# Optimization experiments

Measured on AMD Instinct MI355X. Metric: run time of the kernel, lower is better.

## Reference

```python
import jax, jax.numpy as jnp
import numpy as np

H = 1024
NH = 16
B = 32
S = 4096


def setup_inputs() -> dict:
    key = jax.random.key(0)
    ks = jax.random.split(key, 9)
    std = 0.02
    return {
        "x": jax.random.normal(ks[0], (B, S, H), dtype=jnp.float32),
        "Wq": jax.random.normal(ks[1], (H, H), dtype=jnp.float32) * std,
        "bq": jax.random.normal(ks[2], (H,), dtype=jnp.float32) * std,
        "Wk": jax.random.normal(ks[3], (H, H), dtype=jnp.float32) * std,
        "bk": jax.random.normal(ks[4], (H,), dtype=jnp.float32) * std,
        "Wv": jax.random.normal(ks[5], (H, H), dtype=jnp.float32) * std,
        "bv": jax.random.normal(ks[6], (H,), dtype=jnp.float32) * std,
        "Wo": jax.random.normal(ks[7], (H, H), dtype=jnp.float32) * std,
        "bo": jax.random.normal(ks[8], (H,), dtype=jnp.float32) * std,
        "n_heads": NH,
    }


def reference(x, Wq, bq, Wk, bk, Wv, bv, Wo, bo, n_heads):
    b, s, h = x.shape
    dk = h // n_heads
    scale = dk ** -0.5
    # Q only from last position (decode-style single query)
    q = (x[:, -1, :] @ Wq.T + bq).reshape(b, n_heads, dk)          # (B,H,dk)
    k = (x @ Wk.T + bk).reshape(b, s, n_heads, dk)                 # (B,S,H,dk)
    v = (x @ Wv.T + bv).reshape(b, s, n_heads, dk)
    scores = jnp.einsum('bhd,bshd->bhs', q, k) * scale             # (B,H,S)
    attn = jax.nn.softmax(scores, axis=-1)
    out = jnp.einsum('bhs,bshd->bhd', attn, v).reshape(b, h)       # (B,hidden)
    return out @ Wo.T + bo
```

## Files before the change

kernel.cpp:

```cpp
#include <hip/hip_runtime.h>
#include <hip/hip_bf16.h>

#define B_  32
#define S_  4096
#define H_  1024
#define NH_ 16
#define DK_ 64
#define NCH 32
#define ROWS 128
#define TILE 4
#define NT (ROWS / TILE)

#define Q_OFF  0
#define T_OFF  (Q_OFF + B_*H_)
#define YP_OFF (T_OFF + B_*NH_*H_)
#define ML_OFF (YP_OFF + NCH*B_*NH_*H_)
#define Y2_OFF (ML_OFF + NCH*B_*2*NH_)
#define OP_OFF (Y2_OFF + B_*NH_*H_)

#define DOT4(a, v) ((a).x*(v).x + (a).y*(v).y + (a).z*(v).z + (a).w*(v).w)

typedef float v2f __attribute__((ext_vector_type(2)));
struct alignas(16) F4 { v2f lo, hi; };

__device__ __forceinline__ v2f v2z() { v2f z; z.x = 0.f; z.y = 0.f; return z; }

template <int CTRL>
__device__ __forceinline__ float dppadd(float v) {
  int mv = __builtin_amdgcn_update_dpp(0, __float_as_int(v), CTRL, 0xF, 0xF, true);
  return v + __int_as_float(mv);
}

__global__ __launch_bounds__(256) void k_q(const float* __restrict__ x,
                                           const float* __restrict__ Wq,
                                           const float* __restrict__ bq,
                                           float* __restrict__ q) {
  __shared__ __align__(16) float xl[4 * H_];
  int islab = blockIdx.x, bg = blockIdx.y, tid = threadIdx.x;
  #pragma unroll
  for (int k = 0; k < 4; ++k) {
    int idx4 = k * 256 + tid;
    int bl = idx4 >> 8, col4 = idx4 & 255;
    *(float4*)&xl[bl * H_ + col4 * 4] =
        *(const float4*)(x + (((size_t)(bg * 4 + bl)) * S_ + (S_ - 1)) * H_ + col4 * 4);
  }
  __syncthreads();
  int d = tid >> 2, p = tid & 3;
  int i = islab * 64 + d;
  const float* w = Wq + (size_t)i * H_ + p * 256;
  float acc[4] = {0.f, 0.f, 0.f, 0.f};
  #pragma unroll 4
  for (int jj = 0; jj < 256; jj += 4) {
    float4 wv = *(const float4*)(w + jj);
    #pragma unroll
    for (int bl = 0; bl < 4; ++bl) {
      float4 xv = *(const float4*)&xl[bl * H_ + p * 256 + jj];
      acc[bl] += DOT4(xv, wv);
    }
  }
  #pragma unroll
  for (int bl = 0; bl < 4; ++bl) {
    acc[bl] += __shfl_xor(acc[bl], 1);
    acc[bl] += __shfl_xor(acc[bl], 2);
  }
  if (p == 0) {
    float bias = bq[i];
    #pragma unroll
    for (int bl = 0; bl < 4; ++bl)
      q[(size_t)(bg * 4 + bl) * H_ + i] = acc[bl] + bias;
  }
}

__global__ __launch_bounds__(256) void k_t(const float* __restrict__ q,
                                           const float* __restrict__ Wk,
                                           float* __restrict__ t) {
  __shared__ __align__(16) float qh[B_ * DK_];
  int js = blockIdx.x, h = blockIdx.y, tid = threadIdx.x;
  #pragma unroll
  for (int k = 0; k < 2; ++k) {
    int idx4 = k * 256 + tid;
    int bl = idx4 >> 4, d4 = idx4 & 15;
    *(float4*)&qh[bl * DK_ + d4 * 4] =
        *(const float4*)(q + (size_t)bl * H_ + h * DK_ + d4 * 4);
  }
  __syncthreads();

  int bh = tid >> 7;
  int j = js * 128 + (tid & 127);
  float acc[16];
  #pragma unroll
  for (int bl = 0; bl < 16; ++bl) acc[bl] = 0.f;
  for (int d = 0; d < DK_; ++d) {
    float wv = Wk[((size_t)(h * DK_ + d)) * H_ + j];
    #pragma unroll
    for (int bl = 0; bl < 16; ++bl) acc[bl] += qh[(bh * 16 + bl) * DK_ + d] * wv;
  }
  #pragma unroll
  for (int bl = 0; bl < 16; ++bl)
    t[((size_t)((bh * 16 + bl) * NH_ + h)) * H_ + j] = acc[bl];
}

__global__ __launch_bounds__(256) void k_flash(const float* __restrict__ x,
                                               const float* __restrict__ t,
                                               float* __restrict__ ypart,
                                               float* __restrict__ mlpart) {
  int ch = blockIdx.x, b = blockIdx.y, tid = threadIdx.x;
  int wv = tid >> 6, ln = tid & 63;

  const float* xg = x + ((size_t)b * S_ + (size_t)ch * ROWS) * H_ + ln * 16;

  F4 tf[4][4];
  #pragma unroll
  for (int hh = 0; hh < 4; ++hh) {
    const float* tg = t + ((size_t)b * NH_ + wv * 4 + hh) * H_ + ln * 16;
    #pragma unroll
    for (int j = 0; j < 4; ++j)
      *(float4*)&tf[hh][j] = *(const float4*)(tg + j * 4);
  }

  F4 ya[4][4];
  #pragma unroll
  for (int hh = 0; hh < 4; ++hh)
    #pragma unroll
    for (int j = 0; j < 4; ++j) { ya[hh][j].lo = v2z(); ya[hh][j].hi = v2z(); }
  float m_r[4] = {-3.4e38f, -3.4e38f, -3.4e38f, -3.4e38f};
  float l_r[4] = {0.f, 0.f, 0.f, 0.f};

  #pragma unroll 1
  for (int u = 0; u < NT; ++u) {
    F4 xr[TILE][4];
    #pragma unroll
    for (int s = 0; s < TILE; ++s) {
      const float* xrow = xg + (size_t)(u * TILE + s) * H_;
      #pragma unroll
      for (int j = 0; j < 4; ++j)
        *(float4*)&xr[s][j] = *(const float4*)(xrow + j * 4);
    }

    float scr[4][TILE];
    #pragma unroll
    for (int hh = 0; hh < 4; ++hh)
      #pragma unroll
      for (int s = 0; s < TILE; ++s) {
        v2f a2 = xr[s][0].lo * tf[hh][0].lo;
        a2 += xr[s][0].hi * tf[hh][0].hi;
        a2 += xr[s][1].lo * tf[hh][1].lo;
        a2 += xr[s][1].hi * tf[hh][1].hi;
        a2 += xr[s][2].lo * tf[hh][2].lo;
        a2 += xr[s][2].hi * tf[hh][2].hi;
        a2 += xr[s][3].lo * tf[hh][3].lo;
        a2 += xr[s][3].hi * tf[hh][3].hi;
        scr[hh][s] = a2.x + a2.y;
      }

    #pragma unroll
    for (int hh = 0; hh < 4; ++hh)
      #pragma unroll
      for (int s = 0; s < TILE; ++s) {
        float a = scr[hh][s];
        a = dppadd<0xB1>(a);
        a = dppadd<0x4E>(a);
        a = dppadd<0x141>(a);
        a = dppadd<0x140>(a);
        a += __shfl_xor(a, 16);
        a += __shfl_xor(a, 32);
        scr[hh][s] = a * 0.125f;
      }

    #pragma unroll
    for (int hh = 0; hh < 4; ++hh) {
      float tmax = fmaxf(fmaxf(scr[hh][0], scr[hh][1]), fmaxf(scr[hh][2], scr[hh][3]));
      float mnew = fmaxf(m_r[hh], tmax);
      float fac = __expf(m_r[hh] - mnew);
      float e0 = __expf(scr[hh][0] - mnew);
      float e1 = __expf(scr[hh][1] - mnew);
      float e2 = __expf(scr[hh][2] - mnew);
      float e3 = __expf(scr[hh][3] - mnew);
      m_r[hh] = mnew;
      l_r[hh] = l_r[hh] * fac + (e0 + e1 + e2 + e3);
      #pragma unroll
      for (int j = 0; j < 4; ++j) {
        v2f lo = ya[hh][j].lo * fac;
        lo += e0 * xr[0][j].lo;
        lo += e1 * xr[1][j].lo;
        lo += e2 * xr[2][j].lo;
        lo += e3 * xr[3][j].lo;
        ya[hh][j].lo = lo;
        v2f hi = ya[hh][j].hi * fac;
        hi += e0 * xr[0][j].hi;
        hi += e1 * xr[1][j].hi;
        hi += e2 * xr[2][j].hi;
        hi += e3 * xr[3][j].hi;
        ya[hh][j].hi = hi;
      }
    }
  }

  float* yo = ypart + ((size_t)(ch * B_ + b)) * NH_ * H_ + ln * 16;
  #pragma unroll
  for (int hh = 0; hh < 4; ++hh)
    #pragma unroll
    for (int j = 0; j < 4; ++j)
      *(F4*)(yo + (size_t)(wv * 4 + hh) * H_ + j * 4) = ya[hh][j];
  if (ln == 0) {
    #pragma unroll
    for (int hh = 0; hh < 4; ++hh) {
      size_t base = ((size_t)(ch * B_ + b)) * (2 * NH_) + (size_t)(wv * 4 + hh) * 2;
      mlpart[base + 0] = m_r[hh];
      mlpart[base + 1] = l_r[hh];
    }
  }
}

__global__ __launch_bounds__(256) void k_yred(const float* __restrict__ ypart,
                                              const float* __restrict__ mlpart,
                                              float* __restrict__ y2) {
  int h = blockIdx.x, b = blockIdx.y, tid = threadIdx.x;
  float mg = -3.4e38f;
  for (int ch = 0; ch < NCH; ++ch)
    mg = fmaxf(mg, mlpart[((size_t)(ch * B_ + b)) * (2 * NH_) + h * 2]);
  float L = 0.f;
  float4 acc; acc.x = acc.y = acc.z = acc.w = 0.f;
  for (int ch = 0; ch < NCH; ++ch) {
    float mc = mlpart[((size_t)(ch * B_ + b)) * (2 * NH_) + h * 2 + 0];
    float lc = mlpart[((size_t)(ch * B_ + b)) * (2 * NH_) + h * 2 + 1];
    float w = __expf(mc - mg);
    L += w * lc;
    float4 v = *(const float4*)(ypart +
        ((size_t)(ch * B_ + b)) * NH_ * H_ + (size_t)h * H_ + tid * 4);
    acc.x += w * v.x; acc.y += w * v.y; acc.z += w * v.z; acc.w += w * v.w;
  }
  float inv = 1.f / L;
  acc.x *= inv; acc.y *= inv; acc.z *= inv; acc.w *= inv;
  *(float4*)(y2 + ((size_t)(b * NH_ + h)) * H_ + tid * 4) = acc;
}

__global__ __launch_bounds__(256) void k_vproj(const float* __restrict__ y2,
                                               const float* __restrict__ Wv,
                                               const float* __restrict__ bv,
                                               float* __restrict__ op) {
  __shared__ __align__(16) float yl[4 * H_];
  int h = blockIdx.x, bg = blockIdx.y, tid = threadIdx.x;
  #pragma unroll
  for (int k = 0; k < 4; ++k) {
    int idx4 = k * 256 + tid;
    int bl = idx4 >> 8, col4 = idx4 & 255;
    *(float4*)&yl[bl * H_ + col4 * 4] =
        *(const float4*)(y2 + ((size_t)((bg * 4 + bl) * NH_ + h)) * H_ + col4 * 4);
  }
  __syncthreads();
  int d = tid >> 2, p = tid & 3;
  const float* w = Wv + ((size_t)(h * DK_ + d)) * H_ + p * 256;
  float acc[4] = {0.f, 0.f, 0.f, 0.f};
  #pragma unroll 4
  for (int jj = 0; jj < 256; jj += 4) {
    float4 wv = *(const float4*)(w + jj);
    #pragma unroll
    for (int bl = 0; bl < 4; ++bl) {
      float4 yv = *(const float4*)&yl[bl * H_ + p * 256 + jj];
      acc[bl] += DOT4(yv, wv);
    }
  }
  #pragma unroll
  for (int bl = 0; bl < 4; ++bl) {
    acc[bl] += __shfl_xor(acc[bl], 1);
    acc[bl] += __shfl_xor(acc[bl], 2);
  }
  if (p == 0) {
    float bias = bv[h * DK_ + d];
    #pragma unroll
    for (int bl = 0; bl < 4; ++bl)
      op[(size_t)(bg * 4 + bl) * H_ + h * DK_ + d] = acc[bl] + bias;
  }
}

__global__ __launch_bounds__(256) void k_out(const float* __restrict__ op,
                                             const float* __restrict__ Wo,
                                             const float* __restrict__ bo,
                                             float* __restrict__ out) {
  __shared__ __align__(16) float ul[4 * H_];
  int islab = blockIdx.x, bg = blockIdx.y, tid = threadIdx.x;
  #pragma unroll
  for (int k = 0; k < 4; ++k) {
    int idx4 = k * 256 + tid;
    int bl = idx4 >> 8, col4 = idx4 & 255;
    *(float4*)&ul[bl * H_ + col4 * 4] =
        *(const float4*)(op + (size_t)(bg * 4 + bl) * H_ + col4 * 4);
  }
  __syncthreads();
  int d = tid >> 2, p = tid & 3;
  int i = islab * 64 + d;
  const float* w = Wo + (size_t)i * H_ + p * 256;
  float acc[4] = {0.f, 0.f, 0.f, 0.f};
  #pragma unroll 4
  for (int jj = 0; jj < 256; jj += 4) {
    float4 wv = *(const float4*)(w + jj);
    #pragma unroll
    for (int bl = 0; bl < 4; ++bl) {
      float4 uv = *(const float4*)&ul[bl * H_ + p * 256 + jj];
      acc[bl] += DOT4(uv, wv);
    }
  }
  #pragma unroll
  for (int bl = 0; bl < 4; ++bl) {
    acc[bl] += __shfl_xor(acc[bl], 1);
    acc[bl] += __shfl_xor(acc[bl], 2);
  }
  if (p == 0) {
    float bias = bo[i];
    #pragma unroll
    for (int bl = 0; bl < 4; ++bl)
      out[(size_t)(bg * 4 + bl) * H_ + i] = acc[bl] + bias;
  }
}

extern "C" void kernel_launch(void* const* d_in, const int* in_sizes, int n_in,
                              void* d_out, int out_size, void* d_ws, size_t ws_size,
                              hipStream_t stream) {
  const float* x  = (const float*)d_in[0];
  const float* Wq = (const float*)d_in[1];
  const float* bq = (const float*)d_in[2];
  const float* Wk = (const float*)d_in[3];
  const float* Wv = (const float*)d_in[5];
  const float* bv = (const float*)d_in[6];
  const float* Wo = (const float*)d_in[7];
  const float* bo = (const float*)d_in[8];
  float* out = (float*)d_out;
  float* ws = (float*)d_ws;

  float* q  = ws + Q_OFF;
  float* t  = ws + T_OFF;
  float* yp = ws + YP_OFF;
  float* ml = ws + ML_OFF;
  float* y2 = ws + Y2_OFF;
  float* op = ws + OP_OFF;

  k_q<<<dim3(16, B_ / 4), 256, 0, stream>>>(x, Wq, bq, q);
  k_t<<<dim3(8, NH_), 256, 0, stream>>>(q, Wk, t);
  k_flash<<<dim3(NCH, B_), 256, 0, stream>>>(x, t, yp, ml);
  k_yred<<<dim3(NH_, B_), 256, 0, stream>>>(yp, ml, y2);
  k_vproj<<<dim3(NH_, B_ / 4), 256, 0, stream>>>(y2, Wv, bv, op);
  k_out<<<dim3(16, B_ / 4), 256, 0, stream>>>(op, Wo, bo, out);
}
```

Measured before the change: 273.0 us.

## Stage x tiles through LDS with triple-buffered async global_load_lds pipeline

```diff
diff --git a/kernel.cpp b/kernel.cpp
--- a/kernel.cpp
+++ b/kernel.cpp
@@ -8,8 +8,9 @@
 #define DK_ 64
 #define NCH 32
 #define ROWS 128
-#define TILE 4
+#define TILE 2
 #define NT (ROWS / TILE)
+#define NBUF 3
 
 #define Q_OFF  0
 #define T_OFF  (Q_OFF + B_*H_)
@@ -29,6 +30,12 @@
 __device__ __forceinline__ float dppadd(float v) {
   int mv = __builtin_amdgcn_update_dpp(0, __float_as_int(v), CTRL, 0xF, 0xF, true);
   return v + __int_as_float(mv);
+}
+
+__device__ __forceinline__ void load_lds16(const float* g, float* l) {
+  __builtin_amdgcn_global_load_lds(
+      (const __attribute__((address_space(1))) void*)g,
+      (__attribute__((address_space(3))) void*)l, 16, 0, 0);
 }
 
 __global__ __launch_bounds__(256) void k_q(const float* __restrict__ x,
@@ -104,10 +111,13 @@
                                                const float* __restrict__ t,
                                                float* __restrict__ ypart,
                                                float* __restrict__ mlpart) {
+  __shared__ __align__(16) float xb[NBUF * TILE * H_];
+
   int ch = blockIdx.x, b = blockIdx.y, tid = threadIdx.x;
   int wv = tid >> 6, ln = tid & 63;
 
-  const float* xg = x + ((size_t)b * S_ + (size_t)ch * ROWS) * H_ + ln * 16;
+  const float* xg = x + ((size_t)b * S_ + (size_t)ch * ROWS) * H_;
+  int goff = wv * 256 + ln * 4;
 
   F4 tf[4][4];
   #pragma unroll
@@ -126,16 +136,37 @@
   float m_r[4] = {-3.4e38f, -3.4e38f, -3.4e38f, -3.4e38f};
   float l_r[4] = {0.f, 0.f, 0.f, 0.f};
 
+#define STAGE(tl, bufi)                                                       \
+  {                                                                           \
+    const float* xrow_ = xg + (size_t)(tl) * TILE * H_;                       \
+    _Pragma("unroll") for (int r_ = 0; r_ < TILE; ++r_)                       \
+        load_lds16(xrow_ + (size_t)r_ * H_ + goff,                            \
+                   &xb[(bufi) * (TILE * H_) + r_ * H_ + wv * 256]);           \
+  }
+
+  STAGE(0, 0);
+  STAGE(1, 1);
+
+  int bcur = 0;
   #pragma unroll 1
   for (int u = 0; u < NT; ++u) {
+    if (u >= NT - 1)
+      asm volatile("s_waitcnt vmcnt(0)" ::: "memory");
+    else
+      asm volatile("s_waitcnt vmcnt(2)" ::: "memory");
+    __builtin_amdgcn_s_barrier();
+    __builtin_amdgcn_sched_barrier(0);
+
+    int bn2 = bcur + 2 >= NBUF ? bcur + 2 - NBUF : bcur + 2;
+    if (u + 2 < NT) STAGE(u + 2, bn2);
+
+    const float* xt = &xb[bcur * (TILE * H_)];
     F4 xr[TILE][4];
     #pragma unroll
-    for (int s = 0; s < TILE; ++s) {
-      const float* xrow = xg + (size_t)(u * TILE + s) * H_;
+    for (int s = 0; s < TILE; ++s)
       #pragma unroll
       for (int j = 0; j < 4; ++j)
-        *(float4*)&xr[s][j] = *(const float4*)(xrow + j * 4);
-    }
+        *(float4*)&xr[s][j] = *(const float4*)&xt[s * H_ + ln * 16 + j * 4];
 
     float scr[4][TILE];
     #pragma unroll
@@ -169,32 +200,29 @@
 
     #pragma unroll
     for (int hh = 0; hh < 4; ++hh) {
-      float tmax = fmaxf(fmaxf(scr[hh][0], scr[hh][1]), fmaxf(scr[hh][2], scr[hh][3]));
+      float tmax = fmaxf(scr[hh][0], scr[hh][1]);
       float mnew = fmaxf(m_r[hh], tmax);
       float fac = __expf(m_r[hh] - mnew);
       float e0 = __expf(scr[hh][0] - mnew);
       float e1 = __expf(scr[hh][1] - mnew);
-      float e2 = __expf(scr[hh][2] - mnew);
-      float e3 = __expf(scr[hh][3] - mnew);
       m_r[hh] = mnew;
-      l_r[hh] = l_r[hh] * fac + (e0 + e1 + e2 + e3);
+      l_r[hh] = l_r[hh] * fac + (e0 + e1);
       #pragma unroll
       for (int j = 0; j < 4; ++j) {
         v2f lo = ya[hh][j].lo * fac;
         lo += e0 * xr[0][j].lo;
         lo += e1 * xr[1][j].lo;
-        lo += e2 * xr[2][j].lo;
-        lo += e3 * xr[3][j].lo;
         ya[hh][j].lo = lo;
         v2f hi = ya[hh][j].hi * fac;
         hi += e0 * xr[0][j].hi;
         hi += e1 * xr[1][j].hi;
-        hi += e2 * xr[2][j].hi;
-        hi += e3 * xr[3][j].hi;
         ya[hh][j].hi = hi;
       }
     }
-  }
+
+    bcur = bcur + 1 >= NBUF ? 0 : bcur + 1;
+  }
+#undef STAGE
 
   float* yo = ypart + ((size_t)(ch * B_ + b)) * NH_ * H_ + ln * 16;
   #pragma unroll
```

New measurement: 345.9 us. +26.7%, slower.

## Fuse chunk reduction into V projection and use lazy softmax rescaling

Applied to the files above, without the earlier changes.

```diff
diff --git a/kernel.cpp b/kernel.cpp
--- a/kernel.cpp
+++ b/kernel.cpp
@@ -15,8 +15,7 @@
 #define T_OFF  (Q_OFF + B_*H_)
 #define YP_OFF (T_OFF + B_*NH_*H_)
 #define ML_OFF (YP_OFF + NCH*B_*NH_*H_)
-#define Y2_OFF (ML_OFF + NCH*B_*2*NH_)
-#define OP_OFF (Y2_OFF + B_*NH_*H_)
+#define OP_OFF (ML_OFF + NCH*B_*2*NH_)
 
 #define DOT4(a, v) ((a).x*(v).x + (a).y*(v).y + (a).z*(v).z + (a).w*(v).w)
 
@@ -170,23 +169,31 @@
     #pragma unroll
     for (int hh = 0; hh < 4; ++hh) {
       float tmax = fmaxf(fmaxf(scr[hh][0], scr[hh][1]), fmaxf(scr[hh][2], scr[hh][3]));
-      float mnew = fmaxf(m_r[hh], tmax);
-      float fac = __expf(m_r[hh] - mnew);
-      float e0 = __expf(scr[hh][0] - mnew);
-      float e1 = __expf(scr[hh][1] - mnew);
-      float e2 = __expf(scr[hh][2] - mnew);
-      float e3 = __expf(scr[hh][3] - mnew);
-      m_r[hh] = mnew;
-      l_r[hh] = l_r[hh] * fac + (e0 + e1 + e2 + e3);
+      if (tmax > m_r[hh] + 8.f) {
+        float mnew = tmax;
+        float fac = __expf(m_r[hh] - mnew);
+        m_r[hh] = mnew;
+        l_r[hh] *= fac;
+        #pragma unroll
+        for (int j = 0; j < 4; ++j) {
+          ya[hh][j].lo *= fac;
+          ya[hh][j].hi *= fac;
+        }
+      }
+      float e0 = __expf(scr[hh][0] - m_r[hh]);
+      float e1 = __expf(scr[hh][1] - m_r[hh]);
+      float e2 = __expf(scr[hh][2] - m_r[hh]);
+      float e3 = __expf(scr[hh][3] - m_r[hh]);
+      l_r[hh] += (e0 + e1) + (e2 + e3);
       #pragma unroll
       for (int j = 0; j < 4; ++j) {
-        v2f lo = ya[hh][j].lo * fac;
+        v2f lo = ya[hh][j].lo;
         lo += e0 * xr[0][j].lo;
         lo += e1 * xr[1][j].lo;
         lo += e2 * xr[2][j].lo;
         lo += e3 * xr[3][j].lo;
         ya[hh][j].lo = lo;
-        v2f hi = ya[hh][j].hi * fac;
+        v2f hi = ya[hh][j].hi;
         hi += e0 * xr[0][j].hi;
         hi += e1 * xr[1][j].hi;
         hi += e2 * xr[2][j].hi;
@@ -212,43 +219,37 @@
   }
 }
 
-__global__ __launch_bounds__(256) void k_yred(const float* __restrict__ ypart,
-                                              const float* __restrict__ mlpart,
-                                              float* __restrict__ y2) {
-  int h = blockIdx.x, b = blockIdx.y, tid = threadIdx.x;
-  float mg = -3.4e38f;
-  for (int ch = 0; ch < NCH; ++ch)
-    mg = fmaxf(mg, mlpart[((size_t)(ch * B_ + b)) * (2 * NH_) + h * 2]);
-  float L = 0.f;
-  float4 acc; acc.x = acc.y = acc.z = acc.w = 0.f;
-  for (int ch = 0; ch < NCH; ++ch) {
-    float mc = mlpart[((size_t)(ch * B_ + b)) * (2 * NH_) + h * 2 + 0];
-    float lc = mlpart[((size_t)(ch * B_ + b)) * (2 * NH_) + h * 2 + 1];
-    float w = __expf(mc - mg);
-    L += w * lc;
-    float4 v = *(const float4*)(ypart +
-        ((size_t)(ch * B_ + b)) * NH_ * H_ + (size_t)h * H_ + tid * 4);
-    acc.x += w * v.x; acc.y += w * v.y; acc.z += w * v.z; acc.w += w * v.w;
-  }
-  float inv = 1.f / L;
-  acc.x *= inv; acc.y *= inv; acc.z *= inv; acc.w *= inv;
-  *(float4*)(y2 + ((size_t)(b * NH_ + h)) * H_ + tid * 4) = acc;
-}
-
-__global__ __launch_bounds__(256) void k_vproj(const float* __restrict__ y2,
+__global__ __launch_bounds__(256) void k_vproj(const float* __restrict__ ypart,
+                                               const float* __restrict__ mlpart,
                                                const float* __restrict__ Wv,
                                                const float* __restrict__ bv,
                                                float* __restrict__ op) {
   __shared__ __align__(16) float yl[4 * H_];
   int h = blockIdx.x, bg = blockIdx.y, tid = threadIdx.x;
-  #pragma unroll
-  for (int k = 0; k < 4; ++k) {
-    int idx4 = k * 256 + tid;
-    int bl = idx4 >> 8, col4 = idx4 & 255;
-    *(float4*)&yl[bl * H_ + col4 * 4] =
-        *(const float4*)(y2 + ((size_t)((bg * 4 + bl) * NH_ + h)) * H_ + col4 * 4);
+
+  #pragma unroll
+  for (int bl = 0; bl < 4; ++bl) {
+    int b = bg * 4 + bl;
+    float mg = -3.4e38f;
+    for (int ch = 0; ch < NCH; ++ch)
+      mg = fmaxf(mg, mlpart[((size_t)(ch * B_ + b)) * (2 * NH_) + h * 2]);
+    float L = 0.f;
+    float4 acc; acc.x = acc.y = acc.z = acc.w = 0.f;
+    for (int ch = 0; ch < NCH; ++ch) {
+      float mc = mlpart[((size_t)(ch * B_ + b)) * (2 * NH_) + h * 2 + 0];
+      float lc = mlpart[((size_t)(ch * B_ + b)) * (2 * NH_) + h * 2 + 1];
+      float w = __expf(mc - mg);
+      L += w * lc;
+      float4 v = *(const float4*)(ypart +
+          ((size_t)(ch * B_ + b)) * NH_ * H_ + (size_t)h * H_ + tid * 4);
+      acc.x += w * v.x; acc.y += w * v.y; acc.z += w * v.z; acc.w += w * v.w;
+    }
+    float inv = 1.f / L;
+    acc.x *= inv; acc.y *= inv; acc.z *= inv; acc.w *= inv;
+    *(float4*)&yl[bl * H_ + tid * 4] = acc;
   }
   __syncthreads();
+
   int d = tid >> 2, p = tid & 3;
   const float* w = Wv + ((size_t)(h * DK_ + d)) * H_ + p * 256;
   float acc[4] = {0.f, 0.f, 0.f, 0.f};
@@ -332,13 +333,11 @@
   float* t  = ws + T_OFF;
   float* yp = ws + YP_OFF;
   float* ml = ws + ML_OFF;
-  float* y2 = ws + Y2_OFF;
   float* op = ws + OP_OFF;
 
   k_q<<<dim3(16, B_ / 4), 256, 0, stream>>>(x, Wq, bq, q);
   k_t<<<dim3(8, NH_), 256, 0, stream>>>(q, Wk, t);
   k_flash<<<dim3(NCH, B_), 256, 0, stream>>>(x, t, yp, ml);
-  k_yred<<<dim3(NH_, B_), 256, 0, stream>>>(yp, ml, y2);
-  k_vproj<<<dim3(NH_, B_ / 4), 256, 0, stream>>>(y2, Wv, bv, op);
+  k_vproj<<<dim3(NH_, B_ / 4), 256, 0, stream>>>(yp, ml, Wv, bv, op);
   k_out<<<dim3(16, B_ / 4), 256, 0, stream>>>(op, Wo, bo, out);
 }
```

Measured after the change: 283.3 us. +3.8%, slower.
